# Performance work log

Measured on AMD Instinct MI355X. Metric: run time of the kernel, lower is better.

Reference implementation:

```python
import jax, jax.numpy as jnp
import numpy as np

N_NODES = 100000
ALPHA = 0.01
K_STEPS = 10


def setup_inputs() -> dict:
    key = jax.random.key(0)
    ks = jax.random.split(key, 8)
    n_edges = 1600000
    in_f, hid, out_f = 512, 128, 32
    x = jax.random.normal(ks[0], (N_NODES, in_f), dtype=jnp.float32)
    edge_row = jax.random.randint(ks[1], (n_edges,), 0, N_NODES, dtype=jnp.int64)
    edge_col = jax.random.randint(ks[2], (n_edges,), 0, N_NODES, dtype=jnp.int64)
    # normalized-adjacency-like edge weights, scaled by ~1/avg_degree for stability
    edge_val = jax.random.uniform(ks[3], (n_edges,), dtype=jnp.float32) / 16.0
    W1 = jax.random.normal(ks[4], (in_f, hid), dtype=jnp.float32) / np.sqrt(in_f)
    b1 = jnp.zeros((hid,), dtype=jnp.float32)
    W2 = jax.random.normal(ks[5], (hid, out_f), dtype=jnp.float32) / np.sqrt(hid)
    b2 = jnp.zeros((out_f,), dtype=jnp.float32)
    return {"x": x, "edge_row": edge_row, "edge_col": edge_col, "edge_val": edge_val,
            "W1": W1, "b1": b1, "W2": W2, "b2": b2}


def _spmm(edge_row, edge_col, edge_val, h):
    # out[row] = sum_{edges e with row_e==row} val_e * h[col_e]
    msg = edge_val[:, None] * h[edge_col]  # [E, d]
    return jax.ops.segment_sum(msg, edge_row, num_segments=N_NODES)


def reference(x, edge_row, edge_col, edge_val, W1, b1, W2, b2):
    # MLP (activation after every Linear, as in the original loop)
    h = jax.nn.relu(x @ W1 + b1)
    h = jax.nn.relu(h @ W2 + b2)
    # k-step personalized propagation: h = (1-alpha)*A h + alpha*h
    def step(h, _):
        h = (1.0 - ALPHA) * _spmm(edge_row, edge_col, edge_val, h) + ALPHA * h
        return h, None
    h, _ = jax.lax.scan(step, h, None, length=K_STEPS)
    return h
```

## Files before the change

kernel.cpp:

```cpp
#include <hip/hip_runtime.h>
#include <hip/hip_bf16.h>

#define N_NODES 100000
#define N_EDGES 1600000
#define IN_F 512
#define HID 128
#define OUT_F 32
#define ALPHA 0.01f
#define K_STEPS 10

#define NB 256
#define CH 6250
#define NBUCK 391
#define NS (NBUCK * NB)
#define CAP 5120

typedef __attribute__((ext_vector_type(8))) short short8;
typedef __attribute__((ext_vector_type(4))) float f32x4;
typedef __attribute__((ext_vector_type(8))) _Float16 half8;

__device__ __forceinline__ unsigned short f2bf(float f) {
    union { float f; unsigned u; } c; c.f = f;
    unsigned r = c.u + 0x7FFF + ((c.u >> 16) & 1);
    return (unsigned short)(r >> 16);
}


__launch_bounds__(256)
__global__ void p1_hist_kernel(const int* __restrict__ er, int* __restrict__ S) {
    __shared__ int h[NBUCK];
    int t = threadIdx.x, bl = blockIdx.x;
    for (int b = t; b < NBUCK; b += 256) h[b] = 0;
    __syncthreads();
    int s = bl * CH, e = s + CH;
    for (int i = s + t; i < e; i += 256) atomicAdd(&h[er[i] >> 8], 1);
    __syncthreads();
    for (int b = t; b < NBUCK; b += 256) S[b * NB + bl] = h[b];
}


#define SCAN_B 512
__global__ void scan_block_kernel(const int* __restrict__ cnt, int* __restrict__ partial,
                                  int* __restrict__ bsum, int n) {
    __shared__ int s[SCAN_B];
    int tid = threadIdx.x;
    int i = blockIdx.x * SCAN_B + tid;
    int v = (i < n) ? cnt[i] : 0;
    s[tid] = v;
    __syncthreads();
    for (int off = 1; off < SCAN_B; off <<= 1) {
        int t = (tid >= off) ? s[tid - off] : 0;
        __syncthreads();
        s[tid] += t;
        __syncthreads();
    }
    if (i < n) partial[i] = s[tid];
    if (tid == SCAN_B - 1) bsum[blockIdx.x] = s[tid];
}

__global__ void scan_tops_kernel(int* __restrict__ bsum, int nb) {
    __shared__ int s[256];
    int t = threadIdx.x;
    int v = (t < nb) ? bsum[t] : 0;
    s[t] = v;
    __syncthreads();
    for (int off = 1; off < 256; off <<= 1) {
        int x = (t >= off) ? s[t - off] : 0;
        __syncthreads();
        s[t] += x;
        __syncthreads();
    }
    if (t < nb) bsum[t] = s[t] - v;
}

__global__ void scan_finish_excl_kernel(const int* __restrict__ partial, const int* __restrict__ bsum,
                                        const int* __restrict__ cnt, int* __restrict__ excl, int n) {
    int i = blockIdx.x * blockDim.x + threadIdx.x;
    if (i < n) excl[i] = partial[i] + bsum[i / SCAN_B] - cnt[i];
}


__launch_bounds__(256)
__global__ void p1_scatter_kernel(const int* __restrict__ er, const int* __restrict__ ec,
                                  const float* __restrict__ ev, const int* __restrict__ Sexcl,
                                  int2* __restrict__ sorted) {
    __shared__ int cur[NBUCK];
    int t = threadIdx.x, bl = blockIdx.x;
    for (int b = t; b < NBUCK; b += 256) cur[b] = Sexcl[b * NB + bl];
    __syncthreads();
    int s = bl * CH, e = s + CH;
    for (int i = s + t; i < e; i += 256) {
        int r = er[i];
        int b = r >> 8;
        int pos = atomicAdd(&cur[b], 1);
        sorted[pos] = make_int2(ec[i] | ((r & 255) << 17), __float_as_int(ev[i]));
    }
}


__launch_bounds__(256)
__global__ void p2_build_kernel(const int2* __restrict__ sorted, const int* __restrict__ Sexcl,
                                int* __restrict__ rowptr, int2* __restrict__ edges) {
    __shared__ int rcnt[256], rexcl[256], rcur[256], sc[256];
    __shared__ int2 stage[CAP];
    int t = threadIdx.x, b = blockIdx.x;
    int base = Sexcl[b * NB];
    int end = (b == NBUCK - 1) ? N_EDGES : Sexcl[(b + 1) * NB];
    int cnt = end - base;
    rcnt[t] = 0; rcur[t] = 0;
    __syncthreads();
    for (int i = t; i < cnt; i += 256)
        atomicAdd(&rcnt[((unsigned)sorted[base + i].x) >> 17], 1);
    __syncthreads();
    int v = rcnt[t];
    sc[t] = v;
    __syncthreads();
    for (int off = 1; off < 256; off <<= 1) {
        int x = (t >= off) ? sc[t - off] : 0;
        __syncthreads();
        sc[t] += x;
        __syncthreads();
    }
    rexcl[t] = sc[t] - v;
    int row = (b << 8) + t;
    if (row < N_NODES) rowptr[row] = base + sc[t] - v;
    if (b == NBUCK - 1 && t == 0) rowptr[N_NODES] = N_EDGES;
    __syncthreads();
    for (int i = t; i < cnt; i += 256) {
        int2 ed = sorted[base + i];
        int lr = ((unsigned)ed.x) >> 17;
        int2 o = make_int2(ed.x & 0x1FFFF, ed.y);
        int pos = rexcl[lr] + atomicAdd(&rcur[lr], 1);
        if (pos < CAP) stage[pos] = o;
        else edges[base + pos] = o;
    }
    __syncthreads();
    int lim = cnt < CAP ? cnt : CAP;
    for (int i = t; i < lim; i += 256) edges[base + i] = stage[i];
}


__global__ void wconv_kernel(const float* __restrict__ W1, const float* __restrict__ W2,
                             short* __restrict__ W1T, short* __restrict__ W2T) {
    int idx = blockIdx.x * 256 + threadIdx.x;
    if (idx < IN_F * HID) {
        int k = idx >> 7, nn = idx & 127;
        W1T[nn * IN_F + k] = (short)f2bf(W1[idx]);
    }
    if (idx < HID * OUT_F) {
        int k = idx >> 5, nn = idx & 31;
        W2T[nn * HID + k] = (short)f2bf(W2[idx]);
    }
}


#define AB_PITCH 40
#define H1_PITCH 136

__launch_bounds__(256)
__global__ void mlp_kernel(const float* __restrict__ X, const short* __restrict__ W1T,
                           const float* __restrict__ b1, const short* __restrict__ W2T,
                           const float* __restrict__ b2, _Float16* __restrict__ H, int M) {
    __shared__ char lds[43520];
    short* As  = (short*)lds;
    short* Bs  = (short*)(lds + 10240);
    short* H1s = (short*)lds;
    short* W2s = (short*)(lds + 34816);

    const int t = threadIdx.x;
    const int m0 = blockIdx.x * 128;
    const int l = t & 63;
    const int w = t >> 6;
    const int l15 = l & 15;
    const int koff = (l >> 4) << 3;

    {
        int nn = t >> 3, seg = (t & 7) << 4;
        const short8* src = (const short8*)(W2T + nn * HID + seg);
        *(short8*)&W2s[nn * H1_PITCH + seg] = src[0];
        *(short8*)&W2s[nn * H1_PITCH + seg + 8] = src[1];
    }

    const int arow = t >> 1;
    const int ah = (t & 1) << 4;
    int gm = m0 + arow; if (gm >= M) gm = M - 1;
    const float* xrow = X + (size_t)gm * IN_F;
    const short* wrow = W1T + (size_t)arow * IN_F;

    f32x4 acc[2][8];
    #pragma unroll
    for (int m = 0; m < 2; ++m)
        #pragma unroll
        for (int n = 0; n < 8; ++n) acc[m][n] = (f32x4){0.f, 0.f, 0.f, 0.f};

    for (int k0 = 0; k0 < IN_F; k0 += 32) {
        float4 v0 = *(const float4*)(xrow + k0 + ah);
        float4 v1 = *(const float4*)(xrow + k0 + ah + 4);
        float4 v2 = *(const float4*)(xrow + k0 + ah + 8);
        float4 v3 = *(const float4*)(xrow + k0 + ah + 12);
        short8 p0, p1;
        p0[0] = f2bf(v0.x); p0[1] = f2bf(v0.y); p0[2] = f2bf(v0.z); p0[3] = f2bf(v0.w);
        p0[4] = f2bf(v1.x); p0[5] = f2bf(v1.y); p0[6] = f2bf(v1.z); p0[7] = f2bf(v1.w);
        p1[0] = f2bf(v2.x); p1[1] = f2bf(v2.y); p1[2] = f2bf(v2.z); p1[3] = f2bf(v2.w);
        p1[4] = f2bf(v3.x); p1[5] = f2bf(v3.y); p1[6] = f2bf(v3.z); p1[7] = f2bf(v3.w);
        short8 q0 = *(const short8*)(wrow + k0 + ah);
        short8 q1 = *(const short8*)(wrow + k0 + ah + 8);
        __syncthreads();
        *(short8*)&As[arow * AB_PITCH + ah] = p0;
        *(short8*)&As[arow * AB_PITCH + ah + 8] = p1;
        *(short8*)&Bs[arow * AB_PITCH + ah] = q0;
        *(short8*)&Bs[arow * AB_PITCH + ah + 8] = q1;
        __syncthreads();
        short8 af0 = *(const short8*)&As[(32 * w + l15) * AB_PITCH + koff];
        short8 af1 = *(const short8*)&As[(32 * w + 16 + l15) * AB_PITCH + koff];
        #pragma unroll
        for (int n = 0; n < 8; ++n) {
            short8 bf = *(const short8*)&Bs[(16 * n + l15) * AB_PITCH + koff];
            acc[0][n] = __builtin_amdgcn_mfma_f32_16x16x32_bf16(af0, bf, acc[0][n], 0, 0, 0);
            acc[1][n] = __builtin_amdgcn_mfma_f32_16x16x32_bf16(af1, bf, acc[1][n], 0, 0, 0);
        }
    }

    float bcol[8];
    #pragma unroll
    for (int n = 0; n < 8; ++n) bcol[n] = b1[16 * n + l15];
    __syncthreads();
    #pragma unroll
    for (int m = 0; m < 2; ++m)
        #pragma unroll
        for (int n = 0; n < 8; ++n)
            #pragma unroll
            for (int reg = 0; reg < 4; ++reg) {
                int hrow = 32 * w + 16 * m + ((l >> 4) << 2) + reg;
                float v = fmaxf(acc[m][n][reg] + bcol[n], 0.f);
                H1s[hrow * H1_PITCH + 16 * n + l15] = (short)f2bf(v);
            }
    __syncthreads();

    f32x4 acc2[2][2];
    #pragma unroll
    for (int m = 0; m < 2; ++m)
        #pragma unroll
        for (int n = 0; n < 2; ++n) acc2[m][n] = (f32x4){0.f, 0.f, 0.f, 0.f};
    #pragma unroll
    for (int kc = 0; kc < 4; ++kc) {
        short8 a0 = *(const short8*)&H1s[(32 * w + l15) * H1_PITCH + (kc << 5) + koff];
        short8 a1 = *(const short8*)&H1s[(32 * w + 16 + l15) * H1_PITCH + (kc << 5) + koff];
        #pragma unroll
        for (int n = 0; n < 2; ++n) {
            short8 bf = *(const short8*)&W2s[(16 * n + l15) * H1_PITCH + (kc << 5) + koff];
            acc2[0][n] = __builtin_amdgcn_mfma_f32_16x16x32_bf16(a0, bf, acc2[0][n], 0, 0, 0);
            acc2[1][n] = __builtin_amdgcn_mfma_f32_16x16x32_bf16(a1, bf, acc2[1][n], 0, 0, 0);
        }
    }
    #pragma unroll
    for (int n = 0; n < 2; ++n) {
        float bc = b2[16 * n + l15];
        #pragma unroll
        for (int m = 0; m < 2; ++m)
            #pragma unroll
            for (int reg = 0; reg < 4; ++reg) {
                int row = 32 * w + 16 * m + ((l >> 4) << 2) + reg;
                int g = m0 + row;
                if (g < M)
                    H[(size_t)g * OUT_F + 16 * n + l15] = (_Float16)fmaxf(acc2[m][n][reg] + bc, 0.f);
            }
    }
}


template <int LAST>
__launch_bounds__(256)
__global__ void spmm_kernel(const int* __restrict__ rowptr, const int2* __restrict__ edges,
                            const half8* __restrict__ src, half8* __restrict__ dst,
                            float* __restrict__ dstf, int n) {
    int g = blockIdx.x * 256 + threadIdx.x;
    int r = g >> 2, lane = g & 3;
    if (r >= n) return;
    int s = rowptr[r], e = rowptr[r + 1];
    float a0 = 0.f, a1 = 0.f, a2 = 0.f, a3 = 0.f, a4 = 0.f, a5 = 0.f, a6 = 0.f, a7 = 0.f;
    int i = s;
    for (; i + 4 <= e; i += 4) {
        int2 e0 = edges[i], e1 = edges[i + 1], e2 = edges[i + 2], e3 = edges[i + 3];
        half8 v0 = src[(size_t)e0.x * 4 + lane];
        half8 v1 = src[(size_t)e1.x * 4 + lane];
        half8 v2 = src[(size_t)e2.x * 4 + lane];
        half8 v3 = src[(size_t)e3.x * 4 + lane];
        float w0 = __int_as_float(e0.y), w1 = __int_as_float(e1.y);
        float w2 = __int_as_float(e2.y), w3 = __int_as_float(e3.y);
        a0 = fmaf(w0, (float)v0[0], a0); a1 = fmaf(w0, (float)v0[1], a1);
        a2 = fmaf(w0, (float)v0[2], a2); a3 = fmaf(w0, (float)v0[3], a3);
        a4 = fmaf(w0, (float)v0[4], a4); a5 = fmaf(w0, (float)v0[5], a5);
        a6 = fmaf(w0, (float)v0[6], a6); a7 = fmaf(w0, (float)v0[7], a7);
        a0 = fmaf(w1, (float)v1[0], a0); a1 = fmaf(w1, (float)v1[1], a1);
        a2 = fmaf(w1, (float)v1[2], a2); a3 = fmaf(w1, (float)v1[3], a3);
        a4 = fmaf(w1, (float)v1[4], a4); a5 = fmaf(w1, (float)v1[5], a5);
        a6 = fmaf(w1, (float)v1[6], a6); a7 = fmaf(w1, (float)v1[7], a7);
        a0 = fmaf(w2, (float)v2[0], a0); a1 = fmaf(w2, (float)v2[1], a1);
        a2 = fmaf(w2, (float)v2[2], a2); a3 = fmaf(w2, (float)v2[3], a3);
        a4 = fmaf(w2, (float)v2[4], a4); a5 = fmaf(w2, (float)v2[5], a5);
        a6 = fmaf(w2, (float)v2[6], a6); a7 = fmaf(w2, (float)v2[7], a7);
        a0 = fmaf(w3, (float)v3[0], a0); a1 = fmaf(w3, (float)v3[1], a1);
        a2 = fmaf(w3, (float)v3[2], a2); a3 = fmaf(w3, (float)v3[3], a3);
        a4 = fmaf(w3, (float)v3[4], a4); a5 = fmaf(w3, (float)v3[5], a5);
        a6 = fmaf(w3, (float)v3[6], a6); a7 = fmaf(w3, (float)v3[7], a7);
    }
    for (; i < e; ++i) {
        int2 e0 = edges[i];
        half8 v0 = src[(size_t)e0.x * 4 + lane];
        float w0 = __int_as_float(e0.y);
        a0 = fmaf(w0, (float)v0[0], a0); a1 = fmaf(w0, (float)v0[1], a1);
        a2 = fmaf(w0, (float)v0[2], a2); a3 = fmaf(w0, (float)v0[3], a3);
        a4 = fmaf(w0, (float)v0[4], a4); a5 = fmaf(w0, (float)v0[5], a5);
        a6 = fmaf(w0, (float)v0[6], a6); a7 = fmaf(w0, (float)v0[7], a7);
    }
    half8 self = src[(size_t)r * 4 + lane];
    float r0 = (1.f - ALPHA) * a0 + ALPHA * (float)self[0];
    float r1 = (1.f - ALPHA) * a1 + ALPHA * (float)self[1];
    float r2 = (1.f - ALPHA) * a2 + ALPHA * (float)self[2];
    float r3 = (1.f - ALPHA) * a3 + ALPHA * (float)self[3];
    float r4 = (1.f - ALPHA) * a4 + ALPHA * (float)self[4];
    float r5 = (1.f - ALPHA) * a5 + ALPHA * (float)self[5];
    float r6 = (1.f - ALPHA) * a6 + ALPHA * (float)self[6];
    float r7 = (1.f - ALPHA) * a7 + ALPHA * (float)self[7];
    if (LAST) {
        float* o = dstf + (size_t)r * OUT_F + lane * 8;
        *(float4*)o = make_float4(r0, r1, r2, r3);
        *(float4*)(o + 4) = make_float4(r4, r5, r6, r7);
    } else {
        half8 o;
        o[0] = (_Float16)r0; o[1] = (_Float16)r1; o[2] = (_Float16)r2; o[3] = (_Float16)r3;
        o[4] = (_Float16)r4; o[5] = (_Float16)r5; o[6] = (_Float16)r6; o[7] = (_Float16)r7;
        dst[(size_t)r * 4 + lane] = o;
    }
}


extern "C" void kernel_launch(void* const* d_in, const int* in_sizes, int n_in,
                              void* d_out, int out_size, void* d_ws, size_t ws_size,
                              hipStream_t stream) {
    const float* x  = (const float*)d_in[0];
    const int*   er = (const int*)d_in[1];
    const int*   ec = (const int*)d_in[2];
    const float* ev = (const float*)d_in[3];
    const float* W1 = (const float*)d_in[4];
    const float* b1 = (const float*)d_in[5];
    const float* W2 = (const float*)d_in[6];
    const float* b2 = (const float*)d_in[7];
    float* out = (float*)d_out;

    char* ws = (char*)d_ws;
    _Float16* bufA  = (_Float16*)(ws + 0);
    _Float16* bufB  = (_Float16*)(ws + 6400000);
    int2*  edges  = (int2*) (ws + 12800000);
    int2*  sorted = (int2*) (ws + 25600000);
    short* W1T    = (short*)(ws + 38400000);
    short* W2T    = (short*)(ws + 38531072);
    int*   rowptr = (int*)  (ws + 38539264);
    int*   S      = (int*)  (ws + 38939280);
    int*   Spart  = (int*)  (ws + 39339664);
    int*   Sexcl  = (int*)  (ws + 39740048);
    int*   bsum   = (int*)  (ws + 40140432);

    p1_hist_kernel<<<NB, 256, 0, stream>>>(er, S);
    int nb = (NS + SCAN_B - 1) / SCAN_B;
    scan_block_kernel<<<nb, SCAN_B, 0, stream>>>(S, Spart, bsum, NS);
    scan_tops_kernel<<<1, 256, 0, stream>>>(bsum, nb);
    scan_finish_excl_kernel<<<(NS + 255) / 256, 256, 0, stream>>>(Spart, bsum, S, Sexcl, NS);
    p1_scatter_kernel<<<NB, 256, 0, stream>>>(er, ec, ev, Sexcl, sorted);
    p2_build_kernel<<<NBUCK, 256, 0, stream>>>(sorted, Sexcl, rowptr, edges);

    wconv_kernel<<<(IN_F * HID + 255) / 256, 256, 0, stream>>>(W1, W2, W1T, W2T);

    mlp_kernel<<<(N_NODES + 127) / 128, 256, 0, stream>>>(x, W1T, b1, W2T, b2, bufA, N_NODES);

    _Float16* src = bufA;
    for (int step = 0; step < K_STEPS; ++step) {
        _Float16* dst = (step & 1) ? bufA : bufB;
        int grid = (N_NODES * 4 + 255) / 256;
        if (step == K_STEPS - 1)
            spmm_kernel<1><<<grid, 256, 0, stream>>>(rowptr, edges, (const half8*)src,
                                                     (half8*)dst, out, N_NODES);
        else
            spmm_kernel<0><<<grid, 256, 0, stream>>>(rowptr, edges, (const half8*)src,
                                                     (half8*)dst, nullptr, N_NODES);
        src = dst;
    }
}
```

Measured before the change: 651.0 us.

## Reorder SpMM rows by degree class to balance per-wavefront work

Adds a preprocessing pass that histograms row degrees, scans the histogram and scatters rows into a degree-sorted order (rowinfo holding start, row id and degree). The SpMM kernel then walks rows in that order, so the 16 rows sharing a wavefront have similar edge counts and less lane divergence and tail imbalance. In exchange it adds three small kernels and a memset to the setup path, and it loses row-sequential locality for the self reads and output writes.

```diff
diff --git a/kernel.cpp b/kernel.cpp
--- a/kernel.cpp
+++ b/kernel.cpp
@@ -137,6 +137,65 @@
     __syncthreads();
     int lim = cnt < CAP ? cnt : CAP;
     for (int i = t; i < lim; i += 256) edges[base + i] = stage[i];
+}
+
+
+#define DCLASS 256
+
+__launch_bounds__(256)
+__global__ void deg_hist_kernel(const int* __restrict__ rowptr, int* __restrict__ gh) {
+    __shared__ int h[DCLASS];
+    int t = threadIdx.x;
+    h[t] = 0;
+    __syncthreads();
+    int i = blockIdx.x * 256 + t;
+    if (i < N_NODES) {
+        int d = rowptr[i + 1] - rowptr[i];
+        if (d > 255) d = 255;
+        atomicAdd(&h[d], 1);
+    }
+    __syncthreads();
+    if (h[t]) atomicAdd(&gh[t], h[t]);
+}
+
+__global__ void deg_scan_kernel(int* __restrict__ gh) {
+    __shared__ int s[DCLASS];
+    int t = threadIdx.x;
+    int v = gh[t];
+    s[t] = v;
+    __syncthreads();
+    for (int off = 1; off < 256; off <<= 1) {
+        int x = (t >= off) ? s[t - off] : 0;
+        __syncthreads();
+        s[t] += x;
+        __syncthreads();
+    }
+    gh[t] = s[t] - v;
+}
+
+__launch_bounds__(256)
+__global__ void deg_scatter_kernel(const int* __restrict__ rowptr, const int* __restrict__ gbase,
+                                   int* __restrict__ gcur, int2* __restrict__ rowinfo) {
+    __shared__ int lcnt[DCLASS], lbase[DCLASS], lcur[DCLASS];
+    int t = threadIdx.x;
+    lcnt[t] = 0; lcur[t] = 0;
+    __syncthreads();
+    int i = blockIdx.x * 256 + t;
+    int d = 0, s = 0, dc = 0;
+    bool valid = i < N_NODES;
+    if (valid) {
+        s = rowptr[i];
+        d = rowptr[i + 1] - s;
+        dc = d > 255 ? 255 : d;
+        atomicAdd(&lcnt[dc], 1);
+    }
+    __syncthreads();
+    if (lcnt[t]) lbase[t] = gbase[t] + atomicAdd(&gcur[t], lcnt[t]);
+    __syncthreads();
+    if (valid) {
+        int pos = lbase[dc] + atomicAdd(&lcur[dc], 1);
+        rowinfo[pos] = make_int2(s, i | (d << 17));
+    }
 }
 
 
@@ -271,13 +330,16 @@
 
 template <int LAST>
 __launch_bounds__(256)
-__global__ void spmm_kernel(const int* __restrict__ rowptr, const int2* __restrict__ edges,
+__global__ void spmm_kernel(const int2* __restrict__ rowinfo, const int2* __restrict__ edges,
                             const half8* __restrict__ src, half8* __restrict__ dst,
                             float* __restrict__ dstf, int n) {
     int g = blockIdx.x * 256 + threadIdx.x;
     int r = g >> 2, lane = g & 3;
     if (r >= n) return;
-    int s = rowptr[r], e = rowptr[r + 1];
+    int2 info = rowinfo[r];
+    int s = info.x;
+    int row = info.y & 0x1FFFF;
+    int e = s + (((unsigned)info.y) >> 17);
     float a0 = 0.f, a1 = 0.f, a2 = 0.f, a3 = 0.f, a4 = 0.f, a5 = 0.f, a6 = 0.f, a7 = 0.f;
     int i = s;
     for (; i + 4 <= e; i += 4) {
@@ -314,7 +376,7 @@
         a4 = fmaf(w0, (float)v0[4], a4); a5 = fmaf(w0, (float)v0[5], a5);
         a6 = fmaf(w0, (float)v0[6], a6); a7 = fmaf(w0, (float)v0[7], a7);
     }
-    half8 self = src[(size_t)r * 4 + lane];
+    half8 self = src[(size_t)row * 4 + lane];
     float r0 = (1.f - ALPHA) * a0 + ALPHA * (float)self[0];
     float r1 = (1.f - ALPHA) * a1 + ALPHA * (float)self[1];
     float r2 = (1.f - ALPHA) * a2 + ALPHA * (float)self[2];
@@ -324,14 +386,14 @@
     float r6 = (1.f - ALPHA) * a6 + ALPHA * (float)self[6];
     float r7 = (1.f - ALPHA) * a7 + ALPHA * (float)self[7];
     if (LAST) {
-        float* o = dstf + (size_t)r * OUT_F + lane * 8;
+        float* o = dstf + (size_t)row * OUT_F + lane * 8;
         *(float4*)o = make_float4(r0, r1, r2, r3);
         *(float4*)(o + 4) = make_float4(r4, r5, r6, r7);
     } else {
         half8 o;
         o[0] = (_Float16)r0; o[1] = (_Float16)r1; o[2] = (_Float16)r2; o[3] = (_Float16)r3;
         o[4] = (_Float16)r4; o[5] = (_Float16)r5; o[6] = (_Float16)r6; o[7] = (_Float16)r7;
-        dst[(size_t)r * 4 + lane] = o;
+        dst[(size_t)row * 4 + lane] = o;
     }
 }
 
@@ -352,15 +414,18 @@
     char* ws = (char*)d_ws;
     _Float16* bufA  = (_Float16*)(ws + 0);
     _Float16* bufB  = (_Float16*)(ws + 6400000);
-    int2*  edges  = (int2*) (ws + 12800000);
-    int2*  sorted = (int2*) (ws + 25600000);
-    short* W1T    = (short*)(ws + 38400000);
-    short* W2T    = (short*)(ws + 38531072);
-    int*   rowptr = (int*)  (ws + 38539264);
-    int*   S      = (int*)  (ws + 38939280);
-    int*   Spart  = (int*)  (ws + 39339664);
-    int*   Sexcl  = (int*)  (ws + 39740048);
-    int*   bsum   = (int*)  (ws + 40140432);
+    int2*  edges   = (int2*) (ws + 12800000);
+    int2*  sorted  = (int2*) (ws + 25600000);
+    short* W1T     = (short*)(ws + 38400000);
+    short* W2T     = (short*)(ws + 38531072);
+    int*   rowptr  = (int*)  (ws + 38539264);
+    int*   S       = (int*)  (ws + 38939280);
+    int*   Spart   = (int*)  (ws + 39339664);
+    int*   Sexcl   = (int*)  (ws + 39740048);
+    int*   bsum    = (int*)  (ws + 40140432);
+    int2*  rowinfo = (int2*) (ws + 40141456);
+    int*   gh      = (int*)  (ws + 40941456);
+    int*   gcur    = (int*)  (ws + 40942480);
 
     p1_hist_kernel<<<NB, 256, 0, stream>>>(er, S);
     int nb = (NS + SCAN_B - 1) / SCAN_B;
@@ -370,6 +435,11 @@
     p1_scatter_kernel<<<NB, 256, 0, stream>>>(er, ec, ev, Sexcl, sorted);
     p2_build_kernel<<<NBUCK, 256, 0, stream>>>(sorted, Sexcl, rowptr, edges);
 
+    hipMemsetAsync(gh, 0, 2048, stream);
+    deg_hist_kernel<<<NBUCK, 256, 0, stream>>>(rowptr, gh);
+    deg_scan_kernel<<<1, 256, 0, stream>>>(gh);
+    deg_scatter_kernel<<<NBUCK, 256, 0, stream>>>(rowptr, gh, gcur, rowinfo);
+
     wconv_kernel<<<(IN_F * HID + 255) / 256, 256, 0, stream>>>(W1, W2, W1T, W2T);
 
     mlp_kernel<<<(N_NODES + 127) / 128, 256, 0, stream>>>(x, W1T, b1, W2T, b2, bufA, N_NODES);
@@ -379,10 +449,10 @@
         _Float16* dst = (step & 1) ? bufA : bufB;
         int grid = (N_NODES * 4 + 255) / 256;
         if (step == K_STEPS - 1)
-            spmm_kernel<1><<<grid, 256, 0, stream>>>(rowptr, edges, (const half8*)src,
+            spmm_kernel<1><<<grid, 256, 0, stream>>>(rowinfo, edges, (const half8*)src,
                                                      (half8*)dst, out, N_NODES);
         else
-            spmm_kernel<0><<<grid, 256, 0, stream>>>(rowptr, edges, (const half8*)src,
+            spmm_kernel<0><<<grid, 256, 0, stream>>>(rowinfo, edges, (const half8*)src,
                                                      (half8*)dst, nullptr, N_NODES);
         src = dst;
     }
```

Result: slower. 695.3 us (+6.8%).
